# Kernel optimization log

Measured on AMD Instinct MI355X. Metric: run time of the kernel, lower is better.

## Reference

```python
import jax, jax.numpy as jnp
import numpy as np

B, S, H = 2, 2048, 1024
HFF = 4096
E, K = 8, 2

def setup_inputs() -> dict:
    key = jax.random.key(0)
    k1, k2, k3, k4, k5 = jax.random.split(key, 5)
    x = jax.random.normal(k1, (B, S, H), dtype=jnp.float32)
    topk_probs = jax.random.uniform(k2, (B, S, K), dtype=jnp.float32)
    topk_indices = jax.random.randint(k3, (B, S, K), 0, E, dtype=jnp.int64)
    stdv = 1.0 / np.sqrt(H)
    W1 = jax.random.uniform(k4, (E, HFF, H), minval=-stdv, maxval=stdv, dtype=jnp.float32)
    stdv2 = 1.0 / np.sqrt(HFF)
    W2 = jax.random.uniform(k5, (E, H, HFF), minval=-stdv2, maxval=stdv2, dtype=jnp.float32)
    return {"x": x, "topk_probs": topk_probs, "topk_indices": topk_indices, "W1": W1, "W2": W2}

def reference(x, topk_probs, topk_indices, W1, W2):
    # gate[b,s,e] = max_k topk_probs[b,s,k] * (topk_indices[b,s,k]==e)
    # (max over k, matching probs_mask.max(dim=-1) in the torch module)
    e_ids = jnp.arange(E, dtype=topk_indices.dtype)  # [E]
    sel = topk_indices[..., None] == e_ids  # [B,S,K,E]
    gate = jnp.max(jnp.where(sel, topk_probs[..., None], 0.0), axis=2)  # [B,S,E]
    # dense per-expert FFN over all tokens (as the original computes)
    h = jnp.einsum('bsh,efh->ebsf', x, W1)       # [E,B,S,HFF]
    h = jax.nn.gelu(h)
    y = jnp.einsum('ebsf,ehf->ebsh', h, W2)      # [E,B,S,H]
    # probability applied after FFN, masked combine over experts
    out = jnp.einsum('bse,ebsh->bsh', gate, y)   # [B,S,H]
    return out
```

## Files before the change

kernel.cpp:

```cpp
#include <hip/hip_runtime.h>

typedef unsigned short ushort_t;
typedef __attribute__((ext_vector_type(8))) short short8;
typedef __attribute__((ext_vector_type(4))) float f32x4;

#define TOKENS  4096
#define H_DIM   1024
#define HFF_DIM 4096
#define NEXP    8

__device__ __forceinline__ ushort_t f2b(float f) {
    union { float f; unsigned u; } v; v.f = f;
    unsigned r = v.u + 0x7fffu + ((v.u >> 16) & 1u);
    return (ushort_t)(r >> 16);
}

__device__ __forceinline__ float gelu_tanh(float x) {
    float u = 0.7978845608028654f * (x + 0.044715f * x * x * x);
    return 0.5f * x * (1.0f + tanhf(u));
}

__device__ __forceinline__ void gload16(const ushort_t* g, ushort_t* l) {
    __builtin_amdgcn_global_load_lds(
        (const __attribute__((address_space(1))) unsigned int*)g,
        (__attribute__((address_space(3))) unsigned int*)l,
        16, 0, 0);
}

__global__ void route_kernel(const float* __restrict__ probs,
                             const int* __restrict__ idx,
                             int* __restrict__ count,
                             int* __restrict__ token_id,
                             float* __restrict__ gate) {
    int t = blockIdx.x * blockDim.x + threadIdx.x;
    if (t >= TOKENS) return;
    int i0 = idx[t * 2 + 0];
    int i1 = idx[t * 2 + 1];
    float p0 = probs[t * 2 + 0];
    float p1 = probs[t * 2 + 1];
    if (i0 == i1) {
        float p = fmaxf(p0, p1);
        int pos = atomicAdd(&count[i0], 1);
        token_id[i0 * TOKENS + pos] = t;
        gate[i0 * TOKENS + pos] = p;
    } else {
        int pos = atomicAdd(&count[i0], 1);
        token_id[i0 * TOKENS + pos] = t;
        gate[i0 * TOKENS + pos] = p0;
        pos = atomicAdd(&count[i1], 1);
        token_id[i1 * TOKENS + pos] = t;
        gate[i1 * TOKENS + pos] = p1;
    }
}

__global__ void prefix_kernel(const int* __restrict__ count, int* __restrict__ offsets) {
    if (threadIdx.x == 0 && blockIdx.x == 0) {
        int acc = 0;
        for (int e = 0; e < NEXP; ++e) { offsets[e] = acc; acc += count[e]; }
        offsets[NEXP] = acc;
    }
}

__global__ void cvt_kernel(const float* __restrict__ src, ushort_t* __restrict__ dst, int n8) {
    int i = blockIdx.x * blockDim.x + threadIdx.x;
    if (i >= n8) return;
    const float4* s = (const float4*)(src + (size_t)i * 8);
    float4 a = s[0], b = s[1];
    ushort_t o[8];
    o[0] = f2b(a.x); o[1] = f2b(a.y); o[2] = f2b(a.z); o[3] = f2b(a.w);
    o[4] = f2b(b.x); o[5] = f2b(b.y); o[6] = f2b(b.z); o[7] = f2b(b.w);
    *(short8*)(dst + (size_t)i * 8) = *(short8*)o;
}

__global__ __launch_bounds__(256) void gemm1_kernel(
        const ushort_t* __restrict__ xb, const ushort_t* __restrict__ W1b,
        const int* __restrict__ count, const int* __restrict__ offsets,
        const int* __restrict__ token_id, ushort_t* __restrict__ h) {
    const int wg  = blockIdx.x;
    const int swz = (wg & 7) * (NEXP * 32 * 32 / 8) + (wg >> 3);
    const int e   = swz >> 10;
    const int rem = swz & 1023;
    const int mt  = rem >> 5;
    const int nt  = rem & 31;

    const int cnt = count[e];
    if (mt * 128 >= cnt) return;
    const int base = offsets[e];

    __shared__ __align__(16) ushort_t As[128 * 32];
    __shared__ __align__(16) ushort_t Bs[128 * 32];

    const int tid = threadIdx.x;
    const int lane = tid & 63;
    const int wave = tid >> 6;

    const int sr0 = (wave << 5) + (lane >> 2);
    const int sr1 = sr0 + 16;
    const int sc  = (lane & 3) << 3;

    int ra0 = mt * 128 + sr0; if (ra0 >= cnt) ra0 = cnt - 1;
    int ra1 = mt * 128 + sr1; if (ra1 >= cnt) ra1 = cnt - 1;
    const int t0 = token_id[e * TOKENS + ra0];
    const int t1 = token_id[e * TOKENS + ra1];
    const ushort_t* pa0 = xb + (size_t)t0 * H_DIM + sc;
    const ushort_t* pa1 = xb + (size_t)t1 * H_DIM + sc;
    const ushort_t* pb0 = W1b + (size_t)e * HFF_DIM * H_DIM
                          + (size_t)(nt * 128 + sr0) * H_DIM + sc;
    const ushort_t* pb1 = pb0 + (size_t)16 * H_DIM;
    ushort_t* lA0 = &As[wave << 10];
    ushort_t* lA1 = lA0 + 512;
    ushort_t* lB0 = &Bs[wave << 10];
    ushort_t* lB1 = lB0 + 512;

    const int wm = (wave >> 1) << 6;
    const int wn = (wave & 1) << 6;
    const int lr = lane & 15;
    const int lq = lane >> 4;

    f32x4 acc[4][4];
#pragma unroll
    for (int mi = 0; mi < 4; ++mi)
#pragma unroll
        for (int ni = 0; ni < 4; ++ni)
            acc[mi][ni] = (f32x4){0.f, 0.f, 0.f, 0.f};

    for (int k0 = 0; k0 < H_DIM; k0 += 32) {
        __syncthreads();
        gload16(pa0 + k0, lA0);
        gload16(pa1 + k0, lA1);
        gload16(pb0 + k0, lB0);
        gload16(pb1 + k0, lB1);
        __syncthreads();

        short8 af[4], bf[4];
#pragma unroll
        for (int mi = 0; mi < 4; ++mi)
            af[mi] = *(const short8*)&As[(wm + mi * 16 + lr) * 32 + lq * 8];
#pragma unroll
        for (int ni = 0; ni < 4; ++ni)
            bf[ni] = *(const short8*)&Bs[(wn + ni * 16 + lr) * 32 + lq * 8];
#pragma unroll
        for (int mi = 0; mi < 4; ++mi)
#pragma unroll
            for (int ni = 0; ni < 4; ++ni)
                acc[mi][ni] = __builtin_amdgcn_mfma_f32_16x16x32_bf16(
                    af[mi], bf[ni], acc[mi][ni], 0, 0, 0);
    }

#pragma unroll
    for (int mi = 0; mi < 4; ++mi) {
#pragma unroll
        for (int r = 0; r < 4; ++r) {
            int m = mt * 128 + wm + mi * 16 + lq * 4 + r;
            if (m < cnt) {
                ushort_t* hp = h + (size_t)(base + m) * HFF_DIM + nt * 128 + wn + lr;
#pragma unroll
                for (int ni = 0; ni < 4; ++ni)
                    hp[ni * 16] = f2b(gelu_tanh(acc[mi][ni][r]));
            }
        }
    }
}

__global__ __launch_bounds__(256) void gemm2_kernel(
        const ushort_t* __restrict__ h, const ushort_t* __restrict__ W2b,
        const int* __restrict__ count, const int* __restrict__ offsets,
        const int* __restrict__ token_id, const float* __restrict__ gate,
        float* __restrict__ out) {
    const int wg  = blockIdx.x;
    const int swz = (wg & 7) * (NEXP * 32 * 8 / 8) + (wg >> 3);
    const int e   = swz >> 8;
    const int rem = swz & 255;
    const int mt  = rem >> 3;
    const int nt  = rem & 7;

    const int cnt = count[e];
    if (mt * 128 >= cnt) return;
    const int base = offsets[e];

    __shared__ __align__(16) ushort_t As[128 * 32];
    __shared__ __align__(16) ushort_t Bs[128 * 32];

    const int tid = threadIdx.x;
    const int lane = tid & 63;
    const int wave = tid >> 6;

    const int sr0 = (wave << 5) + (lane >> 2);
    const int sr1 = sr0 + 16;
    const int sc  = (lane & 3) << 3;

    int ra0 = mt * 128 + sr0; if (ra0 >= cnt) ra0 = cnt - 1;
    int ra1 = mt * 128 + sr1; if (ra1 >= cnt) ra1 = cnt - 1;
    const ushort_t* pa0 = h + (size_t)(base + ra0) * HFF_DIM + sc;
    const ushort_t* pa1 = h + (size_t)(base + ra1) * HFF_DIM + sc;
    const ushort_t* pb0 = W2b + (size_t)e * H_DIM * HFF_DIM
                          + (size_t)(nt * 128 + sr0) * HFF_DIM + sc;
    const ushort_t* pb1 = pb0 + (size_t)16 * HFF_DIM;
    ushort_t* lA0 = &As[wave << 10];
    ushort_t* lA1 = lA0 + 512;
    ushort_t* lB0 = &Bs[wave << 10];
    ushort_t* lB1 = lB0 + 512;

    const int wm = (wave >> 1) << 6;
    const int wn = (wave & 1) << 6;
    const int lr = lane & 15;
    const int lq = lane >> 4;

    f32x4 acc[4][4];
#pragma unroll
    for (int mi = 0; mi < 4; ++mi)
#pragma unroll
        for (int ni = 0; ni < 4; ++ni)
            acc[mi][ni] = (f32x4){0.f, 0.f, 0.f, 0.f};

    for (int k0 = 0; k0 < HFF_DIM; k0 += 32) {
        __syncthreads();
        gload16(pa0 + k0, lA0);
        gload16(pa1 + k0, lA1);
        gload16(pb0 + k0, lB0);
        gload16(pb1 + k0, lB1);
        __syncthreads();

        short8 af[4], bf[4];
#pragma unroll
        for (int mi = 0; mi < 4; ++mi)
            af[mi] = *(const short8*)&As[(wm + mi * 16 + lr) * 32 + lq * 8];
#pragma unroll
        for (int ni = 0; ni < 4; ++ni)
            bf[ni] = *(const short8*)&Bs[(wn + ni * 16 + lr) * 32 + lq * 8];
#pragma unroll
        for (int mi = 0; mi < 4; ++mi)
#pragma unroll
            for (int ni = 0; ni < 4; ++ni)
                acc[mi][ni] = __builtin_amdgcn_mfma_f32_16x16x32_bf16(
                    af[mi], bf[ni], acc[mi][ni], 0, 0, 0);
    }

#pragma unroll
    for (int mi = 0; mi < 4; ++mi) {
#pragma unroll
        for (int r = 0; r < 4; ++r) {
            int m = mt * 128 + wm + mi * 16 + lq * 4 + r;
            if (m < cnt) {
                int tok = token_id[e * TOKENS + m];
                float g = gate[e * TOKENS + m];
                float* op = out + (size_t)tok * H_DIM + nt * 128 + wn + lr;
#pragma unroll
                for (int ni = 0; ni < 4; ++ni)
                    atomicAdd(&op[ni * 16], g * acc[mi][ni][r]);
            }
        }
    }
}

extern "C" void kernel_launch(void* const* d_in, const int* in_sizes, int n_in,
                              void* d_out, int out_size, void* d_ws, size_t ws_size,
                              hipStream_t stream) {
    const float* x     = (const float*)d_in[0];
    const float* probs = (const float*)d_in[1];
    const int*   idx   = (const int*)d_in[2];
    const float* W1    = (const float*)d_in[3];
    const float* W2    = (const float*)d_in[4];
    float* out = (float*)d_out;

    char* ws = (char*)d_ws;
    int*      count    = (int*)ws;
    int*      offsets  = (int*)(ws + 64);
    int*      token_id = (int*)(ws + 4096);
    float*    gate     = (float*)(ws + 4096 + 8 * TOKENS * 4);
    ushort_t* xb       = (ushort_t*)(ws + ((size_t)1 << 20));
    ushort_t* Wb       = (ushort_t*)(ws + ((size_t)1 << 20) + ((size_t)8 << 20));
    ushort_t* h        = (ushort_t*)(ws + ((size_t)1 << 20) + ((size_t)72 << 20));

    hipMemsetAsync(count, 0, 64, stream);
    hipMemsetAsync(out, 0, (size_t)out_size * sizeof(float), stream);

    route_kernel<<<TOKENS / 256, 256, 0, stream>>>(probs, idx, count, token_id, gate);
    prefix_kernel<<<1, 64, 0, stream>>>(count, offsets);

    {
        int n8 = TOKENS * H_DIM / 8;
        cvt_kernel<<<(n8 + 255) / 256, 256, 0, stream>>>(x, xb, n8);
    }
    {
        int n8 = NEXP * HFF_DIM * H_DIM / 8;
        cvt_kernel<<<(n8 + 255) / 256, 256, 0, stream>>>(W1, Wb, n8);
    }

    gemm1_kernel<<<NEXP * 32 * 32, 256, 0, stream>>>(xb, Wb, count, offsets, token_id, h);

    {
        int n8 = NEXP * H_DIM * HFF_DIM / 8;
        cvt_kernel<<<(n8 + 255) / 256, 256, 0, stream>>>(W2, Wb, n8);
    }

    gemm2_kernel<<<NEXP * 32 * 8, 256, 0, stream>>>(h, Wb, count, offsets, token_id, gate, out);
}
```

Before: 560.7 us.

## Double the K tile to 64 and XOR-swizzle LDS layout in both GEMMs

Both grouped GEMM kernels now stage a 64-wide K slice per iteration instead of 32, halving the number of barrier pairs per tile. The LDS rows are stored with an XOR swizzle on the 16-byte chunk index (row&7), and fragment reads apply the same swizzle to avoid bank conflicts on the wider 128-byte rows. LDS use doubles to 32KB per block, which may reduce occupancy.

```diff
diff --git a/kernel.cpp b/kernel.cpp
--- a/kernel.cpp
+++ b/kernel.cpp
@@ -72,6 +72,7 @@
     *(short8*)(dst + (size_t)i * 8) = *(short8*)o;
 }
 
+
 __global__ __launch_bounds__(256) void gemm1_kernel(
         const ushort_t* __restrict__ xb, const ushort_t* __restrict__ W1b,
         const int* __restrict__ count, const int* __restrict__ offsets,
@@ -87,35 +88,37 @@
     if (mt * 128 >= cnt) return;
     const int base = offsets[e];
 
-    __shared__ __align__(16) ushort_t As[128 * 32];
-    __shared__ __align__(16) ushort_t Bs[128 * 32];
+    __shared__ __align__(16) ushort_t As[128 * 64];
+    __shared__ __align__(16) ushort_t Bs[128 * 64];
 
     const int tid = threadIdx.x;
     const int lane = tid & 63;
     const int wave = tid >> 6;
 
-    const int sr0 = (wave << 5) + (lane >> 2);
-    const int sr1 = sr0 + 16;
-    const int sc  = (lane & 3) << 3;
-
-    int ra0 = mt * 128 + sr0; if (ra0 >= cnt) ra0 = cnt - 1;
-    int ra1 = mt * 128 + sr1; if (ra1 >= cnt) ra1 = cnt - 1;
-    const int t0 = token_id[e * TOKENS + ra0];
-    const int t1 = token_id[e * TOKENS + ra1];
-    const ushort_t* pa0 = xb + (size_t)t0 * H_DIM + sc;
-    const ushort_t* pa1 = xb + (size_t)t1 * H_DIM + sc;
-    const ushort_t* pb0 = W1b + (size_t)e * HFF_DIM * H_DIM
-                          + (size_t)(nt * 128 + sr0) * H_DIM + sc;
-    const ushort_t* pb1 = pb0 + (size_t)16 * H_DIM;
-    ushort_t* lA0 = &As[wave << 10];
-    ushort_t* lA1 = lA0 + 512;
-    ushort_t* lB0 = &Bs[wave << 10];
-    ushort_t* lB1 = lB0 + 512;
+    const int srow = (lane >> 3);
+    const int sxc  = (((lane & 7) ^ srow) << 3);
+
+    int tok_[4];
+#pragma unroll
+    for (int j = 0; j < 4; ++j) {
+        int ra = mt * 128 + (wave << 5) + j * 8 + srow;
+        if (ra >= cnt) ra = cnt - 1;
+        tok_[j] = token_id[e * TOKENS + ra];
+    }
+    const ushort_t* pa[4];
+    const ushort_t* pb[4];
+#pragma unroll
+    for (int j = 0; j < 4; ++j) {
+        pa[j] = xb + (size_t)tok_[j] * H_DIM + sxc;
+        pb[j] = W1b + (size_t)e * HFF_DIM * H_DIM
+                + (size_t)(nt * 128 + (wave << 5) + j * 8 + srow) * H_DIM + sxc;
+    }
 
     const int wm = (wave >> 1) << 6;
     const int wn = (wave & 1) << 6;
     const int lr = lane & 15;
     const int lq = lane >> 4;
+    const int l7 = lane & 7;
 
     f32x4 acc[4][4];
 #pragma unroll
@@ -124,27 +127,33 @@
         for (int ni = 0; ni < 4; ++ni)
             acc[mi][ni] = (f32x4){0.f, 0.f, 0.f, 0.f};
 
-    for (int k0 = 0; k0 < H_DIM; k0 += 32) {
+    for (int k0 = 0; k0 < H_DIM; k0 += 64) {
         __syncthreads();
-        gload16(pa0 + k0, lA0);
-        gload16(pa1 + k0, lA1);
-        gload16(pb0 + k0, lB0);
-        gload16(pb1 + k0, lB1);
+#pragma unroll
+        for (int j = 0; j < 4; ++j) {
+            gload16(pa[j] + k0, &As[((wave << 5) + j * 8) * 64]);
+            gload16(pb[j] + k0, &Bs[((wave << 5) + j * 8) * 64]);
+        }
         __syncthreads();
 
-        short8 af[4], bf[4];
-#pragma unroll
-        for (int mi = 0; mi < 4; ++mi)
-            af[mi] = *(const short8*)&As[(wm + mi * 16 + lr) * 32 + lq * 8];
-#pragma unroll
-        for (int ni = 0; ni < 4; ++ni)
-            bf[ni] = *(const short8*)&Bs[(wn + ni * 16 + lr) * 32 + lq * 8];
-#pragma unroll
-        for (int mi = 0; mi < 4; ++mi)
+#pragma unroll
+        for (int ks = 0; ks < 2; ++ks) {
+            short8 af[4], bf[4];
+#pragma unroll
+            for (int mi = 0; mi < 4; ++mi)
+                af[mi] = *(const short8*)&As[(wm + mi * 16 + lr) * 64
+                                             + ((((ks << 2) | lq) ^ l7) << 3)];
 #pragma unroll
             for (int ni = 0; ni < 4; ++ni)
-                acc[mi][ni] = __builtin_amdgcn_mfma_f32_16x16x32_bf16(
-                    af[mi], bf[ni], acc[mi][ni], 0, 0, 0);
+                bf[ni] = *(const short8*)&Bs[(wn + ni * 16 + lr) * 64
+                                             + ((((ks << 2) | lq) ^ l7) << 3)];
+#pragma unroll
+            for (int mi = 0; mi < 4; ++mi)
+#pragma unroll
+                for (int ni = 0; ni < 4; ++ni)
+                    acc[mi][ni] = __builtin_amdgcn_mfma_f32_16x16x32_bf16(
+                        af[mi], bf[ni], acc[mi][ni], 0, 0, 0);
+        }
     }
 
 #pragma unroll
@@ -178,33 +187,32 @@
     if (mt * 128 >= cnt) return;
     const int base = offsets[e];
 
-    __shared__ __align__(16) ushort_t As[128 * 32];
-    __shared__ __align__(16) ushort_t Bs[128 * 32];
+    __shared__ __align__(16) ushort_t As[128 * 64];
+    __shared__ __align__(16) ushort_t Bs[128 * 64];
 
     const int tid = threadIdx.x;
     const int lane = tid & 63;
     const int wave = tid >> 6;
 
-    const int sr0 = (wave << 5) + (lane >> 2);
-    const int sr1 = sr0 + 16;
-    const int sc  = (lane & 3) << 3;
-
-    int ra0 = mt * 128 + sr0; if (ra0 >= cnt) ra0 = cnt - 1;
-    int ra1 = mt * 128 + sr1; if (ra1 >= cnt) ra1 = cnt - 1;
-    const ushort_t* pa0 = h + (size_t)(base + ra0) * HFF_DIM + sc;
-    const ushort_t* pa1 = h + (size_t)(base + ra1) * HFF_DIM + sc;
-    const ushort_t* pb0 = W2b + (size_t)e * H_DIM * HFF_DIM
-                          + (size_t)(nt * 128 + sr0) * HFF_DIM + sc;
-    const ushort_t* pb1 = pb0 + (size_t)16 * HFF_DIM;
-    ushort_t* lA0 = &As[wave << 10];
-    ushort_t* lA1 = lA0 + 512;
-    ushort_t* lB0 = &Bs[wave << 10];
-    ushort_t* lB1 = lB0 + 512;
+    const int srow = (lane >> 3);
+    const int sxc  = (((lane & 7) ^ srow) << 3);
+
+    const ushort_t* pa[4];
+    const ushort_t* pb[4];
+#pragma unroll
+    for (int j = 0; j < 4; ++j) {
+        int ra = mt * 128 + (wave << 5) + j * 8 + srow;
+        if (ra >= cnt) ra = cnt - 1;
+        pa[j] = h + (size_t)(base + ra) * HFF_DIM + sxc;
+        pb[j] = W2b + (size_t)e * H_DIM * HFF_DIM
+                + (size_t)(nt * 128 + (wave << 5) + j * 8 + srow) * HFF_DIM + sxc;
+    }
 
     const int wm = (wave >> 1) << 6;
     const int wn = (wave & 1) << 6;
     const int lr = lane & 15;
     const int lq = lane >> 4;
+    const int l7 = lane & 7;
 
     f32x4 acc[4][4];
 #pragma unroll
@@ -213,27 +221,33 @@
         for (int ni = 0; ni < 4; ++ni)
             acc[mi][ni] = (f32x4){0.f, 0.f, 0.f, 0.f};
 
-    for (int k0 = 0; k0 < HFF_DIM; k0 += 32) {
+    for (int k0 = 0; k0 < HFF_DIM; k0 += 64) {
         __syncthreads();
-        gload16(pa0 + k0, lA0);
-        gload16(pa1 + k0, lA1);
-        gload16(pb0 + k0, lB0);
-        gload16(pb1 + k0, lB1);
+#pragma unroll
+        for (int j = 0; j < 4; ++j) {
+            gload16(pa[j] + k0, &As[((wave << 5) + j * 8) * 64]);
+            gload16(pb[j] + k0, &Bs[((wave << 5) + j * 8) * 64]);
+        }
         __syncthreads();
 
-        short8 af[4], bf[4];
-#pragma unroll
-        for (int mi = 0; mi < 4; ++mi)
-            af[mi] = *(const short8*)&As[(wm + mi * 16 + lr) * 32 + lq * 8];
-#pragma unroll
-        for (int ni = 0; ni < 4; ++ni)
-            bf[ni] = *(const short8*)&Bs[(wn + ni * 16 + lr) * 32 + lq * 8];
-#pragma unroll
-        for (int mi = 0; mi < 4; ++mi)
+#pragma unroll
+        for (int ks = 0; ks < 2; ++ks) {
+            short8 af[4], bf[4];
+#pragma unroll
+            for (int mi = 0; mi < 4; ++mi)
+                af[mi] = *(const short8*)&As[(wm + mi * 16 + lr) * 64
+                                             + ((((ks << 2) | lq) ^ l7) << 3)];
 #pragma unroll
             for (int ni = 0; ni < 4; ++ni)
-                acc[mi][ni] = __builtin_amdgcn_mfma_f32_16x16x32_bf16(
-                    af[mi], bf[ni], acc[mi][ni], 0, 0, 0);
+                bf[ni] = *(const short8*)&Bs[(wn + ni * 16 + lr) * 64
+                                             + ((((ks << 2) | lq) ^ l7) << 3)];
+#pragma unroll
+            for (int mi = 0; mi < 4; ++mi)
+#pragma unroll
+                for (int ni = 0; ni < 4; ++ni)
+                    acc[mi][ni] = __builtin_amdgcn_mfma_f32_16x16x32_bf16(
+                        af[mi], bf[ni], acc[mi][ni], 0, 0, 0);
+        }
     }
 
 #pragma unroll
```

New measurement: 605.2 us. 1.08x slower.
